# Performance work log

Hardware: AMD Instinct MI355X
Metric: run time of the kernel (lower is better)

Reference implementation:

```python
import jax, jax.numpy as jnp
import numpy as np

B, H, I = 16384, 512, 256
EPS = 1e-8

def setup_inputs() -> dict:
    key = jax.random.key(0)
    ks = jax.random.split(key, 10)
    x = jax.random.normal(ks[0], (B, I), dtype=jnp.float32)
    hx_re = jax.random.normal(ks[1], (B, H), dtype=jnp.float32) * 0.05
    hx_im = jax.random.normal(ks[2], (B, H), dtype=jnp.float32) * 0.05
    # diag = exp(1j * U(-pi, pi)) -> store angles as real params
    diag_angles = jax.random.uniform(ks[3], (3 * H,), dtype=jnp.float32,
                                     minval=-np.pi, maxval=np.pi)
    # rotation = U(0,1)*2 - (1+1j): real part in [-1,1], imag part in [-1,1]
    rot_re = jax.random.uniform(ks[4], (2 * H,), dtype=jnp.float32) * 2.0 - 1.0
    rot_im = jax.random.uniform(ks[5], (2 * H,), dtype=jnp.float32) * 2.0 - 1.0
    # xavier-scale complex Linear weight (hidden, input), no bias
    w_scale = float(np.sqrt(2.0 / (I + H)))
    W_re = jax.random.normal(ks[6], (H, I), dtype=jnp.float32) * w_scale
    W_im = jax.random.normal(ks[7], (H, I), dtype=jnp.float32) * w_scale
    beta = jnp.zeros((H,), dtype=jnp.float32)  # ModReLU bias, zeros init
    perm = jax.random.permutation(ks[8], H).astype(jnp.int32)
    return {"x": x, "hx_re": hx_re, "hx_im": hx_im,
            "diag_angles": diag_angles, "rot_re": rot_re, "rot_im": rot_im,
            "W_re": W_re, "W_im": W_im, "beta": beta, "perm": perm}

def _unit(v):
    # complex_unit_norm: v / (||v|| + eps), norm over last dim
    return v / (jnp.linalg.norm(v) + EPS)

def _apply_householder(h, v):
    # h @ (I - 2 v v^H) == h - 2 (h @ v) v^H  (rank-1 form, no NxN matrix)
    return h - 2.0 * (h @ v)[:, None] * jnp.conj(v)[None, :]

def reference(x, hx_re, hx_im, diag_angles, rot_re, rot_im, W_re, W_im, beta, perm):
    diag = jnp.exp(1j * diag_angles)                 # complex64, |.| = 1
    d1, d2, d3 = jnp.split(diag, 3)
    rot = rot_re + 1j * rot_im
    r1, r2 = jnp.split(rot, 2)
    v1 = _unit(r1)
    v2 = _unit(r2)

    h = hx_re + 1j * hx_im                           # (B, H) complex64
    h = jnp.fft.fft(d1[None, :] * h, axis=-1)        # D1 then F
    h = _apply_householder(h, v1)                    # R1
    h = jnp.fft.ifft(d2[None, :] * h[:, perm], axis=-1)  # Pi, D2, F^-1
    h = d3[None, :] * _apply_householder(h, v2)      # R2 then D3
    # complex Linear on real input: x @ W^T with complex W
    emb = (x @ W_re.T) + 1j * (x @ W_im.T)
    h = h + emb
    # ModReLU: relu(|z| + beta) * exp(1j * angle(z))
    mag = jnp.abs(h)
    out = jax.nn.relu(mag + beta[None, :]) * jnp.exp(1j * jnp.angle(h))
    # return as real (B, H, 2) [real, imag] for real-valued harness
    return jnp.stack([out.real, out.imag], axis=-1)
```

## Files before the change

### kernel.cpp

```cpp
#include <hip/hip_runtime.h>
#include <hip/hip_bf16.h>
#include <stdint.h>
#include <stddef.h>

typedef __bf16 bf16;
typedef bf16 bf16x8 __attribute__((ext_vector_type(8)));
typedef float f32x4 __attribute__((ext_vector_type(4)));

#define EPSN 1e-8f
#define TWO_PI 6.283185307179586f

#define NB 16384
#define NH 512
#define NI 256
#define KTOT 1280

__device__ __forceinline__ float2 cmul(float2 a, float2 b) {
  return make_float2(a.x * b.x - a.y * b.y, a.x * b.y + a.y * b.x);
}
__device__ __forceinline__ float2 cmulconj(float2 a, float2 b) {
  return make_float2(a.x * b.x + a.y * b.y, a.y * b.x - a.x * b.y);
}
__device__ __forceinline__ float2 cadd(float2 a, float2 b) {
  return make_float2(a.x + b.x, a.y + b.y);
}
__device__ __forceinline__ int brev9(int i) {
  return (int)(__brev((unsigned)i) >> 23);
}

__device__ __forceinline__ void gload16(const bf16* g, bf16* l) {
  __builtin_amdgcn_global_load_lds(
      (const __attribute__((address_space(1))) void*)g,
      (__attribute__((address_space(3))) void*)l, 16, 0, 0);
}

__global__ __launch_bounds__(256) void prep(
    const float* __restrict__ ang, const float* __restrict__ rre,
    const float* __restrict__ rim, const float* __restrict__ wre,
    const float* __restrict__ wim, const int* __restrict__ perm,
    const float* __restrict__ hxre, const float* __restrict__ hxim,
    const float* __restrict__ x, bf16* __restrict__ Bm,
    bf16* __restrict__ Apack) {
  __shared__ float2 bufA[512];
  __shared__ float2 bufB[512];
  __shared__ float2 redw[4];
  __shared__ float2 bc;
  __shared__ float2 red2[256];

  const int bid = blockIdx.x;
  const int t = threadIdx.x;

  if (bid >= 512) {
    const int tid = (bid - 512) * 256 + t;
    const int b = tid / 160;
    const int o = tid - b * 160;
    const float* src;
    if (o < 64)
      src = hxre + (size_t)b * 512 + o * 8;
    else if (o < 128)
      src = hxim + (size_t)b * 512 + (o - 64) * 8;
    else
      src = x + (size_t)b * 256 + (o - 128) * 8;
    float4 f0 = ((const float4*)src)[0];
    float4 f1 = ((const float4*)src)[1];
    bf16x8 v;
    v[0] = (bf16)f0.x; v[1] = (bf16)f0.y; v[2] = (bf16)f0.z; v[3] = (bf16)f0.w;
    v[4] = (bf16)f1.x; v[5] = (bf16)f1.y; v[6] = (bf16)f1.z; v[7] = (bf16)f1.w;
    *(bf16x8*)(Apack + (size_t)b * KTOT + o * 8) = v;
    return;
  }

  const int j = bid;
  const int j0 = t, j1 = t + 256;

  const float r1x0 = rre[j0], r1y0 = rim[j0];
  const float r1x1 = rre[j1], r1y1 = rim[j1];
  const float r2x0 = rre[512 + j0], r2y0 = rim[512 + j0];
  const float r2x1 = rre[512 + j1], r2y1 = rim[512 + j1];
  red2[t] = make_float2(r1x0 * r1x0 + r1y0 * r1y0 + r1x1 * r1x1 + r1y1 * r1y1,
                        r2x0 * r2x0 + r2y0 * r2y0 + r2x1 * r2x1 + r2y1 * r2y1);
  __syncthreads();
  for (int off = 128; off > 0; off >>= 1) {
    if (t < off) {
      red2[t].x += red2[t + off].x;
      red2[t].y += red2[t + off].y;
    }
    __syncthreads();
  }
  const float inv1 = 1.0f / (sqrtf(red2[0].x) + EPSN);
  const float inv2 = 1.0f / (sqrtf(red2[0].y) + EPSN);
  const float2 v1a = make_float2(r1x0 * inv1, r1y0 * inv1);
  const float2 v1b = make_float2(r1x1 * inv1, r1y1 * inv1);
  const float2 v2a = make_float2(r2x0 * inv2, r2y0 * inv2);
  const float2 v2b = make_float2(r2x1 * inv2, r2y1 * inv2);

  {
    float sj, cj;
    __sincosf(ang[j], &sj, &cj);
    const float2 dj = make_float2(cj, sj);
    float2 z = make_float2(0.f, 0.f);
    bufA[brev9(j0)] = (j0 == j) ? dj : z;
    bufA[brev9(j1)] = (j1 == j) ? dj : z;
  }
  __syncthreads();

#pragma unroll
  for (int st = 0; st < 9; ++st) {
    const int half = 1 << st;
    const int pos = t & (half - 1);
    const int i0 = ((t >> st) << (st + 1)) + pos;
    const int i1 = i0 + half;
    const float angv = -TWO_PI * (float)pos / (float)(2 << st);
    float sn, cs;
    __sincosf(angv, &sn, &cs);
    float2 u = bufA[i0];
    float2 w = bufA[i1];
    float2 tw = make_float2(cs * w.x - sn * w.y, cs * w.y + sn * w.x);
    bufA[i0] = make_float2(u.x + tw.x, u.y + tw.y);
    bufA[i1] = make_float2(u.x - tw.x, u.y - tw.y);
    __syncthreads();
  }

  {
    float2 p = cadd(cmul(bufA[j0], v1a), cmul(bufA[j1], v1b));
    for (int off = 32; off > 0; off >>= 1) {
      p.x += __shfl_down(p.x, off);
      p.y += __shfl_down(p.y, off);
    }
    if ((t & 63) == 0) redw[t >> 6] = p;
    __syncthreads();
    if (t == 0) bc = cadd(cadd(redw[0], redw[1]), cadd(redw[2], redw[3]));
    __syncthreads();
  }
  const float2 dot1 = bc;

  {
    float2 c0 = cmulconj(dot1, v1a);
    float2 c1 = cmulconj(dot1, v1b);
    float2 a0 = bufA[j0], a1 = bufA[j1];
    bufA[j0] = make_float2(a0.x - 2.f * c0.x, a0.y - 2.f * c0.y);
    bufA[j1] = make_float2(a1.x - 2.f * c1.x, a1.y - 2.f * c1.y);
  }
  __syncthreads();

  {
    int p0 = perm[j0], p1 = perm[j1];
    float s0, c0, s1, c1;
    __sincosf(ang[512 + j0], &s0, &c0);
    __sincosf(ang[512 + j1], &s1, &c1);
    float2 g0 = cmul(make_float2(c0, s0), bufA[p0]);
    float2 g1 = cmul(make_float2(c1, s1), bufA[p1]);
    bufB[brev9(j0)] = g0;
    bufB[brev9(j1)] = g1;
  }
  __syncthreads();

#pragma unroll
  for (int st = 0; st < 9; ++st) {
    const int half = 1 << st;
    const int pos = t & (half - 1);
    const int i0 = ((t >> st) << (st + 1)) + pos;
    const int i1 = i0 + half;
    const float angv = TWO_PI * (float)pos / (float)(2 << st);
    float sn, cs;
    __sincosf(angv, &sn, &cs);
    float2 u = bufB[i0];
    float2 w = bufB[i1];
    float2 tw = make_float2(cs * w.x - sn * w.y, cs * w.y + sn * w.x);
    bufB[i0] = make_float2(u.x + tw.x, u.y + tw.y);
    bufB[i1] = make_float2(u.x - tw.x, u.y - tw.y);
    __syncthreads();
  }

  {
    float2 q = cadd(cmul(bufB[j0], v2a), cmul(bufB[j1], v2b));
    for (int off = 32; off > 0; off >>= 1) {
      q.x += __shfl_down(q.x, off);
      q.y += __shfl_down(q.y, off);
    }
    if ((t & 63) == 0) redw[t >> 6] = q;
    __syncthreads();
    if (t == 0) bc = cadd(cadd(redw[0], redw[1]), cadd(redw[2], redw[3]));
    __syncthreads();
  }
  const float invN = 1.0f / 512.0f;
  const float2 dot2 = make_float2(bc.x * invN, bc.y * invN);

#pragma unroll
  for (int e = 0; e < 2; ++e) {
    const int i = (e == 0) ? j0 : j1;
    const float2 vj = (e == 0) ? v2a : v2b;
    float2 h2 = make_float2(bufB[i].x * invN, bufB[i].y * invN);
    float2 c2 = cmulconj(dot2, vj);
    float2 hh = make_float2(h2.x - 2.f * c2.x, h2.y - 2.f * c2.y);
    float s3, c3;
    __sincosf(ang[1024 + i], &s3, &c3);
    float2 u = cmul(make_float2(c3, s3), hh);
    bf16* r0 = Bm + (size_t)(2 * i) * KTOT;
    bf16* r1 = Bm + (size_t)(2 * i + 1) * KTOT;
    r0[j] = (bf16)u.x;
    r0[512 + j] = (bf16)(-u.y);
    r1[j] = (bf16)u.y;
    r1[512 + j] = (bf16)u.x;
  }

  Bm[(size_t)(2 * j) * KTOT + 1024 + t] = (bf16)wre[j * NI + t];
  Bm[(size_t)(2 * j + 1) * KTOT + 1024 + t] = (bf16)wim[j * NI + t];
}

__global__ __launch_bounds__(512, 4) void gemm_fused(
    const bf16* __restrict__ Apack, const bf16* __restrict__ Bm,
    const float* __restrict__ beta, float* __restrict__ out) {
  __shared__ bf16 As[128 * 64];
  __shared__ bf16 Bs[128 * 64];

  const int t = threadIdx.x;
  const int lane = t & 63;
  const int wv = t >> 6;

  const int id = blockIdx.x;
  const int xcd = id & 7;
  const int lix = id >> 3;
  const int mBase = (xcd * 16 + (lix >> 3)) * 128;
  const int nBase = (lix & 7) * 128;

  const int subrow = lane >> 3;
  const int soct = (lane & 7) ^ subrow;
  const int srow = wv * 16 + subrow;
  const bf16* gA = Apack + (size_t)(mBase + srow) * KTOT + soct * 8;
  const bf16* gB = Bm + (size_t)(nBase + srow) * KTOT + soct * 8;
  bf16* lA = As + (wv * 16) * 64;
  bf16* lB = Bs + (wv * 16) * 64;

  const int lr = lane & 15;
  const int lq = lane >> 4;
  const int lrm = lr & 7;
  const int waveM = wv & 1;
  const int waveN = wv >> 1;

  f32x4 acc[4][2] = {};

  for (int kk = 0; kk < KTOT; kk += 64) {
    gload16(gA + kk, lA);
    gload16(gA + kk + (size_t)8 * KTOT, lA + 8 * 64);
    gload16(gB + kk, lB);
    gload16(gB + kk + (size_t)8 * KTOT, lB + 8 * 64);
    __syncthreads();

#pragma unroll
    for (int kh = 0; kh < 2; ++kh) {
      const int co = ((kh * 4 + lq) ^ lrm) * 8;
      bf16x8 af[4], bfr[2];
#pragma unroll
      for (int mi = 0; mi < 4; ++mi)
        af[mi] = *(const bf16x8*)(&As[(waveM * 64 + mi * 16 + lr) * 64 + co]);
#pragma unroll
      for (int ni = 0; ni < 2; ++ni)
        bfr[ni] = *(const bf16x8*)(&Bs[(waveN * 32 + ni * 16 + lr) * 64 + co]);
#pragma unroll
      for (int mi = 0; mi < 4; ++mi)
#pragma unroll
        for (int ni = 0; ni < 2; ++ni)
          acc[mi][ni] = __builtin_amdgcn_mfma_f32_16x16x32_bf16(
              af[mi], bfr[ni], acc[mi][ni], 0, 0, 0);
    }
    __syncthreads();
  }

  const int col = lane & 15;
  const int row0 = lq * 4;
  const int parity = lane & 1;
#pragma unroll
  for (int ni = 0; ni < 2; ++ni) {
    const int n = nBase + waveN * 32 + ni * 16 + col;
    const float bet = beta[n >> 1];
#pragma unroll
    for (int mi = 0; mi < 4; ++mi) {
      const int mrow = mBase + waveM * 64 + mi * 16 + row0;
#pragma unroll
      for (int r = 0; r < 4; ++r) {
        float a = acc[mi][ni][r];
        float o = __shfl_xor(a, 1);
        float re = parity ? o : a;
        float im = parity ? a : o;
        float mag2 = re * re + im * im;
        float val;
        if (mag2 > 0.f) {
          float rs = __frsqrt_rn(mag2);
          float s = mag2 * rs + bet;
          val = (s > 0.f) ? (parity ? im : re) * (s * rs) : 0.f;
        } else {
          val = (bet > 0.f && parity == 0) ? bet : 0.f;
        }
        out[(size_t)(mrow + r) * 1024 + n] = val;
      }
    }
  }
}

extern "C" void kernel_launch(void* const* d_in, const int* in_sizes, int n_in,
                              void* d_out, int out_size, void* d_ws,
                              size_t ws_size, hipStream_t stream) {
  const float* x = (const float*)d_in[0];
  const float* hxre = (const float*)d_in[1];
  const float* hxim = (const float*)d_in[2];
  const float* ang = (const float*)d_in[3];
  const float* rre = (const float*)d_in[4];
  const float* rim = (const float*)d_in[5];
  const float* wre = (const float*)d_in[6];
  const float* wim = (const float*)d_in[7];
  const float* beta = (const float*)d_in[8];
  const int* perm = (const int*)d_in[9];

  char* ws = (char*)d_ws;
  bf16* Bm = (bf16*)ws;
  bf16* Apack = (bf16*)(ws + (size_t)1024 * KTOT * 2);

  prep<<<512 + (NB * 160) / 256, 256, 0, stream>>>(ang, rre, rim, wre, wim,
                                                   perm, hxre, hxim, x, Bm,
                                                   Apack);
  gemm_fused<<<1024, 512, 0, stream>>>(Apack, Bm, beta, (float*)d_out);
}
```

Before: 203.5 us.

## Enlarge GEMM tile to 256x256 with double-buffered LDS pipeline

Replaces the 128x128 single-buffered GEMM with a 256x256 tile per block, double-buffered LDS, and an interleaved schedule that issues global-to-LDS loads for upcoming k-tiles between MFMA quadrants, using raw barriers and vmcnt waits plus setprio around MFMA bursts. Each wave now holds a 128x64 accumulator. The aim is to raise arithmetic intensity and hide global load latency behind matrix math. In exchange, grid drops to 256 blocks at occupancy 2 with heavy register and LDS use, so fewer blocks run per CU and the hand-written wait counts must be exactly right.

```diff
diff --git a/kernel.cpp b/kernel.cpp
--- a/kernel.cpp
+++ b/kernel.cpp
@@ -14,6 +14,7 @@
 #define NH 512
 #define NI 256
 #define KTOT 1280
+#define NKT 20
 
 __device__ __forceinline__ float2 cmul(float2 a, float2 b) {
   return make_float2(a.x * b.x - a.y * b.y, a.x * b.y + a.y * b.x);
@@ -208,11 +209,62 @@
   Bm[(size_t)(2 * j + 1) * KTOT + 1024 + t] = (bf16)wim[j * NI + t];
 }
 
-__global__ __launch_bounds__(512, 4) void gemm_fused(
+
+#define BARM() __builtin_amdgcn_s_barrier()
+#define WVM(n) asm volatile("s_waitcnt vmcnt(" #n ")" ::: "memory")
+
+__device__ __forceinline__ void stA(const bf16* gA, bf16* Asb, int wv, int h,
+                                    int kt) {
+  const int r0 = h * 64 + wv * 8;
+  const int r1 = r0 + 128;
+  gload16(gA + (size_t)r0 * KTOT + kt * 64, Asb + r0 * 64);
+  gload16(gA + (size_t)r1 * KTOT + kt * 64, Asb + r1 * 64);
+}
+__device__ __forceinline__ void stB(const bf16* gB, bf16* Bsb, int wv, int h,
+                                    int kt) {
+  const int u0 = wv * 2, u1 = u0 + 1;
+  const int r0 = (u0 >> 2) * 64 + h * 32 + (u0 & 3) * 8;
+  const int r1 = (u1 >> 2) * 64 + h * 32 + (u1 & 3) * 8;
+  gload16(gB + (size_t)r0 * KTOT + kt * 64, Bsb + r0 * 64);
+  gload16(gB + (size_t)r1 * KTOT + kt * 64, Bsb + r1 * 64);
+}
+
+__device__ __forceinline__ void lda(const bf16* Asb, int rowbase,
+                                    const int (&co)[2], bf16x8 (&af)[4][2]) {
+#pragma unroll
+  for (int mi = 0; mi < 4; ++mi)
+#pragma unroll
+    for (int kh = 0; kh < 2; ++kh)
+      af[mi][kh] = *(const bf16x8*)&Asb[(rowbase + mi * 16) * 64 + co[kh]];
+}
+__device__ __forceinline__ void ldb(const bf16* Bsb, int rowbase,
+                                    const int (&co)[2], bf16x8 (&bb)[2][2]) {
+#pragma unroll
+  for (int ni = 0; ni < 2; ++ni)
+#pragma unroll
+    for (int kh = 0; kh < 2; ++kh)
+      bb[ni][kh] = *(const bf16x8*)&Bsb[(rowbase + ni * 16) * 64 + co[kh]];
+}
+__device__ __forceinline__ void mmq(const bf16x8 (&af)[4][2],
+                                    const bf16x8 (&bb)[2][2],
+                                    f32x4 (&acc)[8][4], int mh, int nh) {
+  __builtin_amdgcn_s_setprio(1);
+#pragma unroll
+  for (int mi = 0; mi < 4; ++mi)
+#pragma unroll
+    for (int ni = 0; ni < 2; ++ni)
+#pragma unroll
+      for (int kh = 0; kh < 2; ++kh)
+        acc[mh * 4 + mi][nh * 2 + ni] = __builtin_amdgcn_mfma_f32_16x16x32_bf16(
+            af[mi][kh], bb[ni][kh], acc[mh * 4 + mi][nh * 2 + ni], 0, 0, 0);
+  __builtin_amdgcn_s_setprio(0);
+}
+
+__global__ __launch_bounds__(512, 2) void gemm_fused(
     const bf16* __restrict__ Apack, const bf16* __restrict__ Bm,
     const float* __restrict__ beta, float* __restrict__ out) {
-  __shared__ bf16 As[128 * 64];
-  __shared__ bf16 Bs[128 * 64];
+  __shared__ bf16 As[2][256 * 64];
+  __shared__ bf16 Bs[2][256 * 64];
 
   const int t = threadIdx.x;
   const int lane = t & 63;
@@ -221,16 +273,13 @@
   const int id = blockIdx.x;
   const int xcd = id & 7;
   const int lix = id >> 3;
-  const int mBase = (xcd * 16 + (lix >> 3)) * 128;
-  const int nBase = (lix & 7) * 128;
-
-  const int subrow = lane >> 3;
-  const int soct = (lane & 7) ^ subrow;
-  const int srow = wv * 16 + subrow;
-  const bf16* gA = Apack + (size_t)(mBase + srow) * KTOT + soct * 8;
-  const bf16* gB = Bm + (size_t)(nBase + srow) * KTOT + soct * 8;
-  bf16* lA = As + (wv * 16) * 64;
-  bf16* lB = Bs + (wv * 16) * 64;
+  const int mBase = (xcd * 8 + (lix >> 2)) * 256;
+  const int nBase = (lix & 3) * 256;
+
+  const int sub = lane >> 3;
+  const int chunk = (lane & 7) ^ sub;
+  const bf16* gA = Apack + (size_t)(mBase + sub) * KTOT + chunk * 8;
+  const bf16* gB = Bm + (size_t)(nBase + sub) * KTOT + chunk * 8;
 
   const int lr = lane & 15;
   const int lq = lane >> 4;
@@ -238,48 +287,86 @@
   const int waveM = wv & 1;
   const int waveN = wv >> 1;
 
-  f32x4 acc[4][2] = {};
-
-  for (int kk = 0; kk < KTOT; kk += 64) {
-    gload16(gA + kk, lA);
-    gload16(gA + kk + (size_t)8 * KTOT, lA + 8 * 64);
-    gload16(gB + kk, lB);
-    gload16(gB + kk + (size_t)8 * KTOT, lB + 8 * 64);
-    __syncthreads();
-
-#pragma unroll
-    for (int kh = 0; kh < 2; ++kh) {
-      const int co = ((kh * 4 + lq) ^ lrm) * 8;
-      bf16x8 af[4], bfr[2];
-#pragma unroll
-      for (int mi = 0; mi < 4; ++mi)
-        af[mi] = *(const bf16x8*)(&As[(waveM * 64 + mi * 16 + lr) * 64 + co]);
-#pragma unroll
-      for (int ni = 0; ni < 2; ++ni)
-        bfr[ni] = *(const bf16x8*)(&Bs[(waveN * 32 + ni * 16 + lr) * 64 + co]);
-#pragma unroll
-      for (int mi = 0; mi < 4; ++mi)
-#pragma unroll
-        for (int ni = 0; ni < 2; ++ni)
-          acc[mi][ni] = __builtin_amdgcn_mfma_f32_16x16x32_bf16(
-              af[mi], bfr[ni], acc[mi][ni], 0, 0, 0);
-    }
-    __syncthreads();
-  }
+  const int co[2] = {(lq ^ lrm) * 8, ((4 + lq) ^ lrm) * 8};
+  const int arow = waveM * 128 + lr;
+  const int brow = waveN * 64 + lr;
+
+  f32x4 acc[8][4] = {};
+  bf16x8 af[4][2], b0[2][2], b1[2][2];
+
+  stA(gA, &As[0][0], wv, 0, 0);
+  stB(gB, &Bs[0][0], wv, 0, 0);
+  stA(gA, &As[0][0], wv, 1, 0);
+  stB(gB, &Bs[0][0], wv, 1, 0);
+  stA(gA, &As[1][0], wv, 0, 1);
+  stB(gB, &Bs[1][0], wv, 0, 1);
+  WVM(4);
+  BARM();
+
+  for (int i = 0; i < 10; ++i) {
+    const int t1 = 2 * i + 1;
+    const int t2 = (t1 + 1 < NKT) ? t1 + 1 : NKT - 1;
+    const int t3 = (t1 + 2 < NKT) ? t1 + 2 : NKT - 1;
+
+    lda(&As[0][0], arow, co, af);
+    ldb(&Bs[0][0], brow, co, b0);
+    stA(gA, &As[1][0], wv, 1, t1);
+    BARM();
+    mmq(af, b0, acc, 0, 0);
+    BARM();
+    ldb(&Bs[0][0], brow + 32, co, b1);
+    stB(gB, &Bs[1][0], wv, 1, t1);
+    BARM();
+    mmq(af, b1, acc, 0, 1);
+    BARM();
+    lda(&As[0][0], arow + 64, co, af);
+    stA(gA, &As[0][0], wv, 0, t2);
+    BARM();
+    mmq(af, b0, acc, 1, 0);
+    BARM();
+    stB(gB, &Bs[0][0], wv, 0, t2);
+    BARM();
+    mmq(af, b1, acc, 1, 1);
+    WVM(4);
+    BARM();
+
+    lda(&As[1][0], arow, co, af);
+    ldb(&Bs[1][0], brow, co, b0);
+    stA(gA, &As[0][0], wv, 1, t2);
+    BARM();
+    mmq(af, b0, acc, 0, 0);
+    BARM();
+    ldb(&Bs[1][0], brow + 32, co, b1);
+    stB(gB, &Bs[0][0], wv, 1, t2);
+    BARM();
+    mmq(af, b1, acc, 0, 1);
+    BARM();
+    lda(&As[1][0], arow + 64, co, af);
+    stA(gA, &As[1][0], wv, 0, t3);
+    BARM();
+    mmq(af, b0, acc, 1, 0);
+    BARM();
+    stB(gB, &Bs[1][0], wv, 0, t3);
+    BARM();
+    mmq(af, b1, acc, 1, 1);
+    WVM(4);
+    BARM();
+  }
+  WVM(0);
 
   const int col = lane & 15;
   const int row0 = lq * 4;
   const int parity = lane & 1;
 #pragma unroll
-  for (int ni = 0; ni < 2; ++ni) {
-    const int n = nBase + waveN * 32 + ni * 16 + col;
+  for (int nq = 0; nq < 4; ++nq) {
+    const int n = nBase + waveN * 64 + nq * 16 + col;
     const float bet = beta[n >> 1];
 #pragma unroll
-    for (int mi = 0; mi < 4; ++mi) {
-      const int mrow = mBase + waveM * 64 + mi * 16 + row0;
+    for (int mq = 0; mq < 8; ++mq) {
+      const int mrow = mBase + waveM * 128 + mq * 16 + row0;
 #pragma unroll
       for (int r = 0; r < 4; ++r) {
-        float a = acc[mi][ni][r];
+        float a = acc[mq][nq][r];
         float o = __shfl_xor(a, 1);
         float re = parity ? o : a;
         float im = parity ? a : o;
@@ -319,5 +406,5 @@
   prep<<<512 + (NB * 160) / 256, 256, 0, stream>>>(ang, rre, rim, wre, wim,
                                                    perm, hxre, hxim, x, Bm,
                                                    Apack);
-  gemm_fused<<<1024, 512, 0, stream>>>(Apack, Bm, beta, (float*)d_out);
-}
+  gemm_fused<<<256, 512, 0, stream>>>(Apack, Bm, beta, (float*)d_out);
+}
```

Result: no change. 200.8 us (-1.3%).

## Widen GEMM tile to 128x256 and restructure the bf16 pack blocks

Applied to the files above, without the earlier changes.

The fused GEMM now uses a 128x256 output tile per block, 4x4 MFMA accumulators per wave, and 512 blocks instead of 1024. This cuts redundant A-tile loads and raises MFMA work per LDS fetch. All fragments for both k-halves are loaded before the MFMAs are issued. The prep kernel's packing blocks are split by source array so each block reads contiguous rows with shifts instead of divide-by-160. The costs are more registers and LDS per block, and only 512 blocks, which may reduce occupancy or leave wave-quantization imbalance.

```diff
diff --git a/kernel.cpp b/kernel.cpp
--- a/kernel.cpp
+++ b/kernel.cpp
@@ -14,6 +14,7 @@
 #define NH 512
 #define NI 256
 #define KTOT 1280
+#define NKT 20
 
 __device__ __forceinline__ float2 cmul(float2 a, float2 b) {
   return make_float2(a.x * b.x - a.y * b.y, a.x * b.y + a.y * b.x);
@@ -51,22 +52,33 @@
   const int t = threadIdx.x;
 
   if (bid >= 512) {
-    const int tid = (bid - 512) * 256 + t;
-    const int b = tid / 160;
-    const int o = tid - b * 160;
     const float* src;
-    if (o < 64)
-      src = hxre + (size_t)b * 512 + o * 8;
-    else if (o < 128)
-      src = hxim + (size_t)b * 512 + (o - 64) * 8;
-    else
-      src = x + (size_t)b * 256 + (o - 128) * 8;
+    bf16* dst;
+    if (bid < 512 + 4096) {
+      const int tid = (bid - 512) * 256 + t;
+      const int b = tid >> 6;
+      const int o = (tid & 63) * 8;
+      src = hxre + (size_t)b * 512 + o;
+      dst = Apack + (size_t)b * KTOT + o;
+    } else if (bid < 512 + 8192) {
+      const int tid = (bid - 512 - 4096) * 256 + t;
+      const int b = tid >> 6;
+      const int o = (tid & 63) * 8;
+      src = hxim + (size_t)b * 512 + o;
+      dst = Apack + (size_t)b * KTOT + 512 + o;
+    } else {
+      const int tid = (bid - 512 - 8192) * 256 + t;
+      const int b = tid >> 5;
+      const int o = (tid & 31) * 8;
+      src = x + (size_t)b * 256 + o;
+      dst = Apack + (size_t)b * KTOT + 1024 + o;
+    }
     float4 f0 = ((const float4*)src)[0];
     float4 f1 = ((const float4*)src)[1];
     bf16x8 v;
     v[0] = (bf16)f0.x; v[1] = (bf16)f0.y; v[2] = (bf16)f0.z; v[3] = (bf16)f0.w;
     v[4] = (bf16)f1.x; v[5] = (bf16)f1.y; v[6] = (bf16)f1.z; v[7] = (bf16)f1.w;
-    *(bf16x8*)(Apack + (size_t)b * KTOT + o * 8) = v;
+    *(bf16x8*)dst = v;
     return;
   }
 
@@ -212,7 +224,7 @@
     const bf16* __restrict__ Apack, const bf16* __restrict__ Bm,
     const float* __restrict__ beta, float* __restrict__ out) {
   __shared__ bf16 As[128 * 64];
-  __shared__ bf16 Bs[128 * 64];
+  __shared__ bf16 Bs[256 * 64];
 
   const int t = threadIdx.x;
   const int lane = t & 63;
@@ -221,16 +233,13 @@
   const int id = blockIdx.x;
   const int xcd = id & 7;
   const int lix = id >> 3;
-  const int mBase = (xcd * 16 + (lix >> 3)) * 128;
-  const int nBase = (lix & 7) * 128;
-
-  const int subrow = lane >> 3;
-  const int soct = (lane & 7) ^ subrow;
-  const int srow = wv * 16 + subrow;
-  const bf16* gA = Apack + (size_t)(mBase + srow) * KTOT + soct * 8;
-  const bf16* gB = Bm + (size_t)(nBase + srow) * KTOT + soct * 8;
-  bf16* lA = As + (wv * 16) * 64;
-  bf16* lB = Bs + (wv * 16) * 64;
+  const int mBase = (xcd * 16 + (lix >> 2)) * 128;
+  const int nBase = (lix & 3) * 256;
+
+  const int sub = lane >> 3;
+  const int chunk = (lane & 7) ^ sub;
+  const bf16* gA = Apack + (size_t)(mBase + sub) * KTOT + chunk * 8;
+  const bf16* gB = Bm + (size_t)(nBase + sub) * KTOT + chunk * 8;
 
   const int lr = lane & 15;
   const int lq = lane >> 4;
@@ -238,32 +247,42 @@
   const int waveM = wv & 1;
   const int waveN = wv >> 1;
 
-  f32x4 acc[4][2] = {};
-
-  for (int kk = 0; kk < KTOT; kk += 64) {
-    gload16(gA + kk, lA);
-    gload16(gA + kk + (size_t)8 * KTOT, lA + 8 * 64);
-    gload16(gB + kk, lB);
-    gload16(gB + kk + (size_t)8 * KTOT, lB + 8 * 64);
-    __syncthreads();
-
-#pragma unroll
-    for (int kh = 0; kh < 2; ++kh) {
-      const int co = ((kh * 4 + lq) ^ lrm) * 8;
-      bf16x8 af[4], bfr[2];
+  const int co[2] = {(lq ^ lrm) * 8, ((4 + lq) ^ lrm) * 8};
+  const int arow = waveM * 64 + lr;
+  const int brow = waveN * 64 + lr;
+
+  f32x4 acc[4][4] = {};
+
+  for (int kt = 0; kt < NKT; ++kt) {
+    const int ko = kt * 64;
+    gload16(gA + (size_t)(wv * 16) * KTOT + ko, As + (wv * 16) * 64);
+    gload16(gA + (size_t)(wv * 16 + 8) * KTOT + ko, As + (wv * 16 + 8) * 64);
+#pragma unroll
+    for (int j = 0; j < 4; ++j)
+      gload16(gB + (size_t)(wv * 32 + j * 8) * KTOT + ko,
+              Bs + (wv * 32 + j * 8) * 64);
+    __syncthreads();
+
+    bf16x8 af[4][2], bfr[4][2];
+#pragma unroll
+    for (int mi = 0; mi < 4; ++mi)
+#pragma unroll
+      for (int kh = 0; kh < 2; ++kh)
+        af[mi][kh] = *(const bf16x8*)&As[(arow + mi * 16) * 64 + co[kh]];
+#pragma unroll
+    for (int ni = 0; ni < 4; ++ni)
+#pragma unroll
+      for (int kh = 0; kh < 2; ++kh)
+        bfr[ni][kh] = *(const bf16x8*)&Bs[(brow + ni * 16) * 64 + co[kh]];
+
+#pragma unroll
+    for (int kh = 0; kh < 2; ++kh)
 #pragma unroll
       for (int mi = 0; mi < 4; ++mi)
-        af[mi] = *(const bf16x8*)(&As[(waveM * 64 + mi * 16 + lr) * 64 + co]);
-#pragma unroll
-      for (int ni = 0; ni < 2; ++ni)
-        bfr[ni] = *(const bf16x8*)(&Bs[(waveN * 32 + ni * 16 + lr) * 64 + co]);
-#pragma unroll
-      for (int mi = 0; mi < 4; ++mi)
-#pragma unroll
-        for (int ni = 0; ni < 2; ++ni)
+#pragma unroll
+        for (int ni = 0; ni < 4; ++ni)
           acc[mi][ni] = __builtin_amdgcn_mfma_f32_16x16x32_bf16(
-              af[mi], bfr[ni], acc[mi][ni], 0, 0, 0);
-    }
+              af[mi][kh], bfr[ni][kh], acc[mi][ni], 0, 0, 0);
     __syncthreads();
   }
 
@@ -271,8 +290,8 @@
   const int row0 = lq * 4;
   const int parity = lane & 1;
 #pragma unroll
-  for (int ni = 0; ni < 2; ++ni) {
-    const int n = nBase + waveN * 32 + ni * 16 + col;
+  for (int ni = 0; ni < 4; ++ni) {
+    const int n = nBase + waveN * 64 + ni * 16 + col;
     const float bet = beta[n >> 1];
 #pragma unroll
     for (int mi = 0; mi < 4; ++mi) {
@@ -316,8 +335,8 @@
   bf16* Bm = (bf16*)ws;
   bf16* Apack = (bf16*)(ws + (size_t)1024 * KTOT * 2);
 
-  prep<<<512 + (NB * 160) / 256, 256, 0, stream>>>(ang, rre, rim, wre, wim,
-                                                   perm, hxre, hxim, x, Bm,
-                                                   Apack);
-  gemm_fused<<<1024, 512, 0, stream>>>(Apack, Bm, beta, (float*)d_out);
-}
+  prep<<<512 + 4096 + 4096 + 2048, 256, 0, stream>>>(ang, rre, rim, wre, wim,
+                                                     perm, hxre, hxim, x, Bm,
+                                                     Apack);
+  gemm_fused<<<512, 512, 0, stream>>>(Apack, Bm, beta, (float*)d_out);
+}
```

New measurement: 197.4 us. -3.0%, faster.
